# Kernel optimization log

Measured on AMD Instinct MI355X. Metric: run time of the kernel, lower is better.

## Reference

```python
import jax, jax.numpy as jnp
import numpy as np

DIM = 128
NHEADS = 8
N = 4096
ALPHA = 0.2  # LeakyReLU negative slope
EPS = 1e-5   # LayerNorm eps


def setup_inputs() -> dict:
    key = jax.random.key(0)
    ks = jax.random.split(key, 8)
    s = 1.0 / np.sqrt(DIM)
    nodes = jax.random.normal(ks[0], (N, DIM), dtype=jnp.float32)
    adj = jax.random.randint(ks[1], (N, N), 0, 2, dtype=jnp.int32)
    # per-head GAT params: W [H,D,D], attention vectors a1,a2 [H,D]
    W = jax.random.normal(ks[2], (NHEADS, DIM, DIM), dtype=jnp.float32) * s
    a1 = jax.random.normal(ks[3], (NHEADS, DIM), dtype=jnp.float32) * s
    a2 = jax.random.normal(ks[4], (NHEADS, DIM), dtype=jnp.float32) * s
    # linear1: (dim*nheads) -> dim
    W1 = jax.random.normal(ks[5], (NHEADS * DIM, DIM), dtype=jnp.float32) * (1.0 / np.sqrt(NHEADS * DIM))
    b1 = jnp.zeros((DIM,), dtype=jnp.float32)
    gamma = jnp.ones((DIM,), dtype=jnp.float32)
    beta = jnp.zeros((DIM,), dtype=jnp.float32)
    return {"nodes": nodes, "adj": adj, "W": W, "a1": a1, "a2": a2,
            "W1": W1, "b1": b1, "gamma": gamma, "beta": beta}


def _layernorm(x, gamma, beta):
    mu = jnp.mean(x, axis=-1, keepdims=True)
    var = jnp.mean((x - mu) ** 2, axis=-1, keepdims=True)
    return (x - mu) * jax.lax.rsqrt(var + EPS) * gamma + beta


def reference(nodes, adj, W, a1, a2, W1, b1, gamma, beta):
    # Eval mode: all dropouts are identity.
    # Multi-head GAT: Wh [H, N, D]
    Wh = jnp.einsum('nd,hde->hne', nodes, W)
    f1 = jnp.einsum('hnd,hd->hn', Wh, a1)   # [H, N]
    f2 = jnp.einsum('hnd,hd->hn', Wh, a2)   # [H, N]
    e = jax.nn.leaky_relu(f1[:, :, None] + f2[:, None, :], negative_slope=ALPHA)  # [H,N,N]
    mask = (adj > 0)[None, :, :]
    att = jnp.where(mask, e, jnp.float32(-9e15))
    att = jax.nn.softmax(att, axis=-1)
    h = jnp.einsum('hnm,hmd->hnd', att, Wh)  # [H, N, D]
    h = jax.nn.elu(h)
    # concat heads along feature dim -> [N, H*D]
    cat = jnp.transpose(h, (1, 0, 2)).reshape(N, NHEADS * DIM)
    x = jax.nn.elu(cat @ W1 + b1)            # [N, D]
    out = _layernorm(nodes + x, gamma, beta)
    return out
```

## Files before the change

kernel.cpp:

```cpp
#include <hip/hip_runtime.h>
#include <hip/hip_bf16.h>


#define NN 4096
#define ALPHA 0.2f
#define EPSLN 1e-5f
#define LOG2E 1.4426950408889634f

typedef __attribute__((ext_vector_type(8))) _Float16 f16x8;
typedef __attribute__((ext_vector_type(4))) _Float16 f16x4;
typedef __attribute__((ext_vector_type(2))) _Float16 f16x2;
typedef __attribute__((ext_vector_type(4))) float f32x4;
typedef __attribute__((ext_vector_type(4))) int i32x4;
typedef __fp16 h16x2 __attribute__((ext_vector_type(2)));

union F16x8 { f16x8 v; f16x2 h[4]; unsigned u[4]; };
union F16x4 { f16x4 v; f16x2 h[2]; };
union PKU { f16x2 f; unsigned u; h16x2 r; };

static __device__ inline f16x2 pkrtz(float a, float b) {
  union { decltype(__builtin_amdgcn_cvt_pkrtz(0.f, 0.f)) r; f16x2 h; } u;
  u.r = __builtin_amdgcn_cvt_pkrtz(a, b);
  return u.h;
}

#if __has_builtin(__builtin_amdgcn_exp2f)
#define EXP2(x) __builtin_amdgcn_exp2f(x)
#else
#define EXP2(x) exp2f(x)
#endif

static __device__ __forceinline__ unsigned pk_mul(unsigned a, unsigned b) {
  unsigned d;
  asm("v_pk_mul_f16 %0, %1, %2" : "=v"(d) : "v"(a), "v"(b));
  return d;
}
static __device__ __forceinline__ unsigned pk_max(unsigned a, unsigned b) {
  unsigned d;
  asm("v_pk_max_f16 %0, %1, %2" : "=v"(d) : "v"(a), "v"(b));
  return d;
}

static __device__ __forceinline__ float fdot2u(unsigned a, unsigned b, float c) {
#if __has_builtin(__builtin_amdgcn_fdot2)
  PKU ua, ub; ua.u = a; ub.u = b;
  return __builtin_amdgcn_fdot2(ua.r, ub.r, c, false);
#else
  PKU ua, ub; ua.u = a; ub.u = b;
  return c + (float)ua.f[0] * (float)ub.f[0] + (float)ua.f[1] * (float)ub.f[1];
#endif
}

static __device__ __forceinline__ void gload16(const void* g, void* l) {
  __builtin_amdgcn_global_load_lds(
      (const __attribute__((address_space(1))) void*)g,
      (__attribute__((address_space(3))) void*)l, 16, 0, 0);
}

static __device__ inline unsigned long long sp4(unsigned long long x) {
  x = (x | (x << 24)) & 0x000000FF000000FFULL;
  x = (x | (x << 12)) & 0x000F000F000F000FULL;
  x = (x | (x << 6))  & 0x0303030303030303ULL;
  x = (x | (x << 3))  & 0x1111111111111111ULL;
  return x;
}

__global__ void k_packprep(const int* __restrict__ adj, unsigned long long* __restrict__ maskT,
                           const float* __restrict__ W, const float* __restrict__ W1,
                           _Float16* __restrict__ Wt, _Float16* __restrict__ W1t) {
  int bid = blockIdx.x;
  if (bid < 16384) {
    int wv = threadIdx.x >> 6, l = threadIdx.x & 63;
    int gid = bid * 4 + wv;
    int row = gid >> 4, chunk = gid & 15;
    i32x4 v = *(const i32x4*)(adj + ((size_t)row << 12) + chunk * 256 + l * 4);
    unsigned long long b0 = __ballot(v.x > 0);
    unsigned long long b1 = __ballot(v.y > 0);
    unsigned long long b2 = __ballot(v.z > 0);
    unsigned long long b3 = __ballot(v.w > 0);
    if (l < 4) {
      int sh = l * 16;
      unsigned long long w = sp4((b0 >> sh) & 0xFFFF)
                           | (sp4((b1 >> sh) & 0xFFFF) << 1)
                           | (sp4((b2 >> sh) & 0xFFFF) << 2)
                           | (sp4((b3 >> sh) & 0xFFFF) << 3);
      maskT[(size_t)(chunk * 4 + l) * NN + row] = w;
    }
  } else {
    int idx = (bid - 16384) * 256 + threadIdx.x;
    if (idx < 131072) {
      int h = idx >> 14, r = idx & 16383, d = r >> 7, e = r & 127;
      Wt[h * 16384 + e * 128 + d] = (_Float16)W[idx];
    } else {
      int j = idx - 131072;
      int k = j >> 7, d = j & 127;
      W1t[d * 1024 + k] = (_Float16)W1[j];
    }
  }
}

__global__ __launch_bounds__(256) void k_wh(const float* __restrict__ nodes,
    const _Float16* __restrict__ Wt, const float* __restrict__ a1,
    const float* __restrict__ a2, _Float16* __restrict__ Whbt,
    float* __restrict__ f1L, float* __restrict__ f2L) {
  int h = blockIdx.y;
  int wv = threadIdx.x >> 6, l = threadIdx.x & 63;
  int lr = l & 15, lg = l >> 4;
  int ibase = blockIdx.x * 64 + wv * 16;
  f32x4 acc[8] = {};
  const float* arow = nodes + (size_t)(ibase + lr) * 128;
  const _Float16* bbase = Wt + h * 16384;
#pragma unroll
  for (int ks = 0; ks < 4; ++ks) {
    int k0 = ks * 32 + lg * 8;
    f32x4 av0 = *(const f32x4*)(arow + k0);
    f32x4 av1 = *(const f32x4*)(arow + k0 + 4);
    F16x8 A;
    A.h[0] = pkrtz(av0[0], av0[1]);
    A.h[1] = pkrtz(av0[2], av0[3]);
    A.h[2] = pkrtz(av1[0], av1[1]);
    A.h[3] = pkrtz(av1[2], av1[3]);
#pragma unroll
    for (int nt = 0; nt < 8; ++nt) {
      f16x8 B = *(const f16x8*)(bbase + (nt * 16 + lr) * 128 + k0);
      acc[nt] = __builtin_amdgcn_mfma_f32_16x16x32_f16(A.v, B, acc[nt], 0, 0, 0);
    }
  }
#pragma unroll
  for (int nt = 0; nt < 8; ++nt) {
    F16x4 o;
    o.h[0] = pkrtz(acc[nt][0], acc[nt][1]);
    o.h[1] = pkrtz(acc[nt][2], acc[nt][3]);
    *(f16x4*)(Whbt + (size_t)(h * 128 + nt * 16 + lr) * NN + ibase + lg * 4) = o.v;
  }
  float a1r[8], a2r[8];
#pragma unroll
  for (int nt = 0; nt < 8; ++nt) {
    a1r[nt] = a1[h * 128 + nt * 16 + lr];
    a2r[nt] = a2[h * 128 + nt * 16 + lr];
  }
#pragma unroll
  for (int r = 0; r < 4; ++r) {
    float s1 = 0.f, s2 = 0.f;
#pragma unroll
    for (int nt = 0; nt < 8; ++nt) { s1 += acc[nt][r] * a1r[nt]; s2 += acc[nt][r] * a2r[nt]; }
    s1 += __shfl_xor(s1, 1, 16); s1 += __shfl_xor(s1, 2, 16);
    s1 += __shfl_xor(s1, 4, 16); s1 += __shfl_xor(s1, 8, 16);
    s2 += __shfl_xor(s2, 1, 16); s2 += __shfl_xor(s2, 2, 16);
    s2 += __shfl_xor(s2, 4, 16); s2 += __shfl_xor(s2, 8, 16);
    if (lr == 0) {
      int i = ibase + lg * 4 + r;
      f1L[h * NN + i] = s1 * LOG2E;
      f2L[h * NN + i] = s2 * LOG2E;
    }
  }
}

__global__ __launch_bounds__(1024) void k_m2(const float* __restrict__ f2L,
    float* __restrict__ M2L, _Float16* __restrict__ e2ph) {
  __shared__ float red[16];
  int h = blockIdx.x, t = threadIdx.x;
  float a[4];
#pragma unroll
  for (int i = 0; i < 4; ++i) a[i] = f2L[h * NN + t + i * 1024];
  float v = fmaxf(fmaxf(a[0], a[1]), fmaxf(a[2], a[3]));
#pragma unroll
  for (int off = 1; off < 64; off <<= 1) v = fmaxf(v, __shfl_xor(v, off, 64));
  if ((t & 63) == 0) red[t >> 6] = v;
  __syncthreads();
  if (t < 16) {
    float m = red[t];
#pragma unroll
    for (int off = 1; off < 16; off <<= 1) m = fmaxf(m, __shfl_xor(m, off, 16));
    if (t == 0) { red[0] = m; M2L[h] = m; }
  }
  __syncthreads();
  float M2 = red[0];
#pragma unroll
  for (int i = 0; i < 4; ++i) {
    float d = a[i] - M2;
    e2ph[h * 8192 + t + i * 1024] = (_Float16)EXP2(d);
    e2ph[h * 8192 + 4096 + t + i * 1024] = (_Float16)EXP2(ALPHA * d);
  }
}

__global__ __launch_bounds__(256, 2) void k_attn(const _Float16* __restrict__ Whbt,
    const float* __restrict__ f1L, const float* __restrict__ M2L,
    const _Float16* __restrict__ e2ph, const unsigned long long* __restrict__ maskT,
    _Float16* __restrict__ hcat) {
  __shared__ __align__(16) char Bt[2][32768];
  __shared__ __align__(16) _Float16 e2s[2][256];
  __shared__ float denL[4][64];
  int t = threadIdx.x, jq = t >> 6, l = t & 63, lr = l & 15, lg = l >> 4;
  int bid = blockIdx.x;
  int h = bid & 7;
  int rowbase = (bid >> 3) * 64;
  float M2 = M2L[h];
  unsigned E1u[4], Eau[4];
  int rg[4];
#pragma unroll
  for (int g = 0; g < 4; ++g) {
    rg[g] = rowbase + g * 16 + lr;
    float f1 = f1L[h * NN + rg[g]];
    float s = f1 + M2;
    float mL = fmaxf(s, ALPHA * s);
    float e1 = EXP2(s - mL), ea = EXP2(ALPHA * s - mL);
    PKU p1; p1.f = pkrtz(e1, e1); E1u[g] = p1.u;
    PKU p2; p2.f = pkrtz(ea, ea); Eau[g] = p2.u;
  }
  f32x4 acc[4][8] = {};
  float den[4] = {};
  const _Float16* src = Whbt + ((size_t)h << 19);
  const _Float16* ept = e2ph + h * 8192;

  int t4 = t >> 4;
  int jc = (t & 15) ^ (t4 & 15);
  size_t goff = (size_t)t4 * NN + jc * 8;
  size_t gE = (size_t)(((t >> 4) & 1) * 4096) + (t & 15) * 8;
  int mshift = (jq & 1) * 32 + lg * 8;
  int wbase = jq >> 1;

  unsigned long long mc[4];
#pragma unroll
  for (int g = 0; g < 4; ++g) mc[g] = maskT[(size_t)wbase * NN + rg[g]];
  {
    const _Float16* gp = src + goff;
    char* lb = &Bt[0][0] + t * 16;
#pragma unroll
    for (int p = 0; p < 8; ++p)
      gload16(gp + (size_t)p * 16 * NN, lb + p * 4096);
    if (t < 32) gload16(ept + gE, (char*)&e2s[0][0] + t * 16);
  }
  __syncthreads();

  for (int ct = 0; ct < 32; ++ct) {
    unsigned long long mn[4] = {};
    if (ct + 1 < 32) {
#pragma unroll
      for (int g = 0; g < 4; ++g)
        mn[g] = maskT[(size_t)((ct + 1) * 2 + wbase) * NN + rg[g]];
      const _Float16* gp = src + goff + (ct + 1) * 128;
      char* lb = &Bt[(ct + 1) & 1][0] + t * 16;
#pragma unroll
      for (int p = 0; p < 8; ++p)
        gload16(gp + (size_t)p * 16 * NN, lb + p * 4096);
      if (t < 32) gload16(ept + gE + (ct + 1) * 128, (char*)&e2s[(ct + 1) & 1][0] + t * 16);
    }
    const char* btr = &Bt[ct & 1][0];
    const char* e2p = (const char*)&e2s[ct & 1][0];
    i32x4 e2w = *(const i32x4*)(e2p + jq * 64 + lg * 16);
    i32x4 e2aw = *(const i32x4*)(e2p + 256 + jq * 64 + lg * 16);
    F16x8 afr[4];
#pragma unroll
    for (int g = 0; g < 4; ++g) {
      unsigned bits = (unsigned)(mc[g] >> mshift) & 0xFFu;
      float dg = den[g];
#pragma unroll
      for (int pi = 0; pi < 4; ++pi) {
        unsigned mx = pk_max(pk_mul(E1u[g], (unsigned)e2w[pi]),
                             pk_mul(Eau[g], (unsigned)e2aw[pi]));
        unsigned b = (bits >> (2 * pi)) & 3u;
        mx &= ((b & 1u) ? 0x0000FFFFu : 0u) | ((b & 2u) ? 0xFFFF0000u : 0u);
        afr[g].u[pi] = mx;
        dg = fdot2u(mx, 0x3C003C00u, dg);
      }
      den[g] = dg;
    }
    __builtin_amdgcn_s_setprio(1);
#pragma unroll
    for (int nt = 0; nt < 8; ++nt) {
      int d = nt * 16 + lr;
      int byteoff = d * 256 + (((jq * 4 + lg) ^ lr) << 4);
      f16x8 B = *(const f16x8*)(btr + byteoff);
#pragma unroll
      for (int g = 0; g < 4; ++g)
        acc[g][nt] = __builtin_amdgcn_mfma_f32_16x16x32_f16(afr[g].v, B, acc[g][nt], 0, 0, 0);
    }
    __builtin_amdgcn_s_setprio(0);
    __syncthreads();
#pragma unroll
    for (int g = 0; g < 4; ++g) mc[g] = mn[g];
  }
#pragma unroll
  for (int g = 0; g < 4; ++g) {
    den[g] += __shfl_xor(den[g], 16, 64);
    den[g] += __shfl_xor(den[g], 32, 64);
  }
  if (l < 16) {
#pragma unroll
    for (int g = 0; g < 4; ++g) denL[jq][g * 16 + lr] = den[g];
  }

  float* cmb = (float*)Bt;
#pragma unroll
  for (int ph = 0; ph < 4; ++ph) {
    if (jq == ph) {
      if (ph == 0) {
#pragma unroll
        for (int g = 0; g < 4; ++g)
#pragma unroll
          for (int nt = 0; nt < 8; ++nt)
#pragma unroll
            for (int r = 0; r < 4; ++r)
              cmb[(g * 16 + lg * 4 + r) * 132 + nt * 16 + lr] = acc[g][nt][r];
      } else {
#pragma unroll
        for (int g = 0; g < 4; ++g)
#pragma unroll
          for (int nt = 0; nt < 8; ++nt)
#pragma unroll
            for (int r = 0; r < 4; ++r)
              cmb[(g * 16 + lg * 4 + r) * 132 + nt * 16 + lr] += acc[g][nt][r];
      }
    }
    __syncthreads();
  }
  {
    int row = t >> 2, seg = t & 3;
    const float* rgp = cmb + row * 132 + seg * 32;
    float dsum = denL[0][row] + denL[1][row] + denL[2][row] + denL[3][row];
    float rc = __builtin_amdgcn_rcpf(dsum);
    _Float16* outp = hcat + (size_t)(rowbase + row) * 1024 + h * 128 + seg * 32;
#pragma unroll
    for (int q8 = 0; q8 < 4; ++q8) {
      f32x4 va = *(const f32x4*)(rgp + q8 * 8);
      f32x4 vb = *(const f32x4*)(rgp + q8 * 8 + 4);
      float x[8];
#pragma unroll
      for (int c = 0; c < 4; ++c) { x[c] = va[c] * rc; x[4 + c] = vb[c] * rc; }
#pragma unroll
      for (int c = 0; c < 8; ++c) x[c] = x[c] > 0.f ? x[c] : EXP2(x[c] * LOG2E) - 1.f;
      F16x8 o;
      o.h[0] = pkrtz(x[0], x[1]); o.h[1] = pkrtz(x[2], x[3]);
      o.h[2] = pkrtz(x[4], x[5]); o.h[3] = pkrtz(x[6], x[7]);
      *(f16x8*)(outp + q8 * 8) = o.v;
    }
  }
}

__global__ __launch_bounds__(256) void k_out(const _Float16* __restrict__ hcat,
    const _Float16* __restrict__ W1t, const float* __restrict__ b1,
    const float* __restrict__ nodes, const float* __restrict__ gamma,
    const float* __restrict__ beta, float* __restrict__ out) {
  __shared__ __align__(16) float part[4][16][132];
  int t = threadIdx.x, w = t >> 6, l = t & 63, lr = l & 15, lg = l >> 4;
  int ibase = blockIdx.x * 16;
  f32x4 acc[8] = {};
  const _Float16* arow = hcat + (size_t)(ibase + lr) * 1024 + w * 256;
  const _Float16* bb = W1t + w * 256;
#pragma unroll
  for (int ks = 0; ks < 8; ++ks) {
    int k0 = ks * 32 + lg * 8;
    f16x8 A = *(const f16x8*)(arow + k0);
#pragma unroll
    for (int nt = 0; nt < 8; ++nt) {
      f16x8 B = *(const f16x8*)(bb + (nt * 16 + lr) * 1024 + k0);
      acc[nt] = __builtin_amdgcn_mfma_f32_16x16x32_f16(A, B, acc[nt], 0, 0, 0);
    }
  }
#pragma unroll
  for (int nt = 0; nt < 8; ++nt)
#pragma unroll
    for (int r = 0; r < 4; ++r)
      part[w][lg * 4 + r][nt * 16 + lr] = acc[nt][r];
  __syncthreads();
  int row = t >> 4, c16 = t & 15;
  int d0 = c16 * 8;
  size_t gi = (size_t)(ibase + row) * 128;
  f32x4 pa = {}, pb = {};
#pragma unroll
  for (int q = 0; q < 4; ++q) {
    pa += *(const f32x4*)&part[q][row][d0];
    pb += *(const f32x4*)&part[q][row][d0 + 4];
  }
  f32x4 ba = *(const f32x4*)(b1 + d0), bbv = *(const f32x4*)(b1 + d0 + 4);
  f32x4 na = *(const f32x4*)(nodes + gi + d0), nb = *(const f32x4*)(nodes + gi + d0 + 4);
  float y[8];
  float sum = 0.f, sq = 0.f;
#pragma unroll
  for (int c = 0; c < 4; ++c) {
    float x = pa[c] + ba[c];
    x = x > 0.f ? x : EXP2(x * LOG2E) - 1.f;
    y[c] = x + na[c];
    float x2 = pb[c] + bbv[c];
    x2 = x2 > 0.f ? x2 : EXP2(x2 * LOG2E) - 1.f;
    y[4 + c] = x2 + nb[c];
  }
#pragma unroll
  for (int c = 0; c < 8; ++c) { sum += y[c]; sq += y[c] * y[c]; }
#pragma unroll
  for (int off = 1; off < 16; off <<= 1) {
    sum += __shfl_xor(sum, off, 16);
    sq += __shfl_xor(sq, off, 16);
  }
  float mu = sum * (1.f / 128.f);
  float var = sq * (1.f / 128.f) - mu * mu;
  float rs = __builtin_amdgcn_rsqf(var + EPSLN);
  f32x4 ga = *(const f32x4*)(gamma + d0), gb = *(const f32x4*)(gamma + d0 + 4);
  f32x4 bea = *(const f32x4*)(beta + d0), beb = *(const f32x4*)(beta + d0 + 4);
  f32x4 o0, o1;
#pragma unroll
  for (int c = 0; c < 4; ++c) {
    o0[c] = (y[c] - mu) * rs * ga[c] + bea[c];
    o1[c] = (y[4 + c] - mu) * rs * gb[c] + beb[c];
  }
  *(f32x4*)(out + gi + d0) = o0;
  *(f32x4*)(out + gi + d0 + 4) = o1;
}

extern "C" void kernel_launch(void* const* d_in, const int* in_sizes, int n_in,
                              void* d_out, int out_size, void* d_ws, size_t ws_size,
                              hipStream_t stream) {
  const float* nodes = (const float*)d_in[0];
  const int* adj = (const int*)d_in[1];
  const float* W = (const float*)d_in[2];
  const float* a1 = (const float*)d_in[3];
  const float* a2 = (const float*)d_in[4];
  const float* W1 = (const float*)d_in[5];
  const float* b1 = (const float*)d_in[6];
  const float* gamma = (const float*)d_in[7];
  const float* beta = (const float*)d_in[8];
  float* out = (float*)d_out;
  char* ws = (char*)d_ws;

  const size_t OFF_MASK = 0;
  const size_t OFF_WHBT = 2097152;
  const size_t OFF_F1 = OFF_WHBT + 8388608;
  const size_t OFF_F2 = OFF_F1 + 131072;
  const size_t OFF_M2 = OFF_F2 + 131072;
  const size_t OFF_E2T = OFF_M2 + 256;
  const size_t OFF_WT = OFF_E2T + 131072;
  const size_t OFF_W1T = OFF_WT + 262144;
  const size_t OFF_HCAT = OFF_W1T + 262144;

  unsigned long long* maskT = (unsigned long long*)(ws + OFF_MASK);
  _Float16* Whbt = (_Float16*)(ws + OFF_WHBT);
  float* f1L = (float*)(ws + OFF_F1);
  float* f2L = (float*)(ws + OFF_F2);
  float* M2L = (float*)(ws + OFF_M2);
  _Float16* e2ph = (_Float16*)(ws + OFF_E2T);
  _Float16* Wt = (_Float16*)(ws + OFF_WT);
  _Float16* W1t = (_Float16*)(ws + OFF_W1T);
  _Float16* hcat = (_Float16*)(ws + OFF_HCAT);

  k_packprep<<<17408, 256, 0, stream>>>(adj, maskT, W, W1, Wt, W1t);
  k_wh<<<dim3(64, 8), 256, 0, stream>>>(nodes, Wt, a1, a2, Whbt, f1L, f2L);
  k_m2<<<8, 1024, 0, stream>>>(f2L, M2L, e2ph);
  k_attn<<<512, 256, 0, stream>>>(Whbt, f1L, M2L, e2ph, maskT, hcat);
  k_out<<<256, 256, 0, stream>>>(hcat, W1t, b1, nodes, gamma, beta, out);
}
```

Measured before the change: 92.90 us.

## Enlarge attention tile to 128 rows and 256-column K-chunks with 512-thread blocks

The attention kernel now uses 512-thread blocks that each cover 128 query rows, split as two row halves by four K-quarter waves. Each K-chunk grows to 256 columns, and the XOR swizzle on the shared-memory Wh tile is adjusted to match. Every loaded Wh tile is now reused across twice as many rows, and the loop runs half as many iterations with half as many barriers. In exchange, the block uses about 128KB of LDS double buffer, which probably allows only one block per CU despite the launch bound of 2. The grid also drops to 256 blocks, which lowers occupancy and latency hiding.

```diff
diff --git a/kernel.cpp b/kernel.cpp
--- a/kernel.cpp
+++ b/kernel.cpp
@@ -184,23 +184,24 @@
   }
 }
 
-__global__ __launch_bounds__(256, 2) void k_attn(const _Float16* __restrict__ Whbt,
+__global__ __launch_bounds__(512, 2) void k_attn(const _Float16* __restrict__ Whbt,
     const float* __restrict__ f1L, const float* __restrict__ M2L,
     const _Float16* __restrict__ e2ph, const unsigned long long* __restrict__ maskT,
     _Float16* __restrict__ hcat) {
-  __shared__ __align__(16) char Bt[2][32768];
-  __shared__ __align__(16) _Float16 e2s[2][256];
-  __shared__ float denL[4][64];
-  int t = threadIdx.x, jq = t >> 6, l = t & 63, lr = l & 15, lg = l >> 4;
+  __shared__ __align__(16) char Bt[2][65536];
+  __shared__ __align__(16) _Float16 e2s[2][512];
+  __shared__ float denL[4][128];
+  int t = threadIdx.x, w = t >> 6, l = t & 63, lr = l & 15, lg = l >> 4;
+  int rh = w >> 2, q = w & 3;
   int bid = blockIdx.x;
   int h = bid & 7;
-  int rowbase = (bid >> 3) * 64;
+  int rowbase = (bid >> 3) * 128;
   float M2 = M2L[h];
   unsigned E1u[4], Eau[4];
   int rg[4];
 #pragma unroll
   for (int g = 0; g < 4; ++g) {
-    rg[g] = rowbase + g * 16 + lr;
+    rg[g] = rowbase + rh * 64 + g * 16 + lr;
     float f1 = f1L[h * NN + rg[g]];
     float s = f1 + M2;
     float mL = fmaxf(s, ALPHA * s);
@@ -213,70 +214,76 @@
   const _Float16* src = Whbt + ((size_t)h << 19);
   const _Float16* ept = e2ph + h * 8192;
 
-  int t4 = t >> 4;
-  int jc = (t & 15) ^ (t4 & 15);
-  size_t goff = (size_t)t4 * NN + jc * 8;
-  size_t gE = (size_t)(((t >> 4) & 1) * 4096) + (t & 15) * 8;
-  int mshift = (jq & 1) * 32 + lg * 8;
-  int wbase = jq >> 1;
+  int tr = t >> 5;
+  int jc0 = (t & 31) ^ tr;
+  const _Float16* gp[8];
+#pragma unroll
+  for (int p = 0; p < 8; ++p) {
+    int jc = jc0 ^ ((p & 1) << 4);
+    gp[p] = src + ((size_t)(p * 16 + tr) << 12) + jc * 8;
+  }
+  const _Float16* egp = ept + ((t >> 5) & 1) * 4096 + (t & 31) * 8;
 
   unsigned long long mc[4];
 #pragma unroll
-  for (int g = 0; g < 4; ++g) mc[g] = maskT[(size_t)wbase * NN + rg[g]];
+  for (int g = 0; g < 4; ++g) mc[g] = maskT[(size_t)q * NN + rg[g]];
   {
-    const _Float16* gp = src + goff;
     char* lb = &Bt[0][0] + t * 16;
 #pragma unroll
-    for (int p = 0; p < 8; ++p)
-      gload16(gp + (size_t)p * 16 * NN, lb + p * 4096);
-    if (t < 32) gload16(ept + gE, (char*)&e2s[0][0] + t * 16);
+    for (int p = 0; p < 8; ++p) gload16(gp[p], lb + p * 8192);
+    if (t < 64) gload16(egp, (char*)&e2s[0][0] + t * 16);
   }
   __syncthreads();
 
-  for (int ct = 0; ct < 32; ++ct) {
+#pragma unroll 2
+  for (int ct = 0; ct < 16; ++ct) {
+    int cur = ct & 1;
     unsigned long long mn[4] = {};
-    if (ct + 1 < 32) {
+    if (ct + 1 < 16) {
 #pragma unroll
       for (int g = 0; g < 4; ++g)
-        mn[g] = maskT[(size_t)((ct + 1) * 2 + wbase) * NN + rg[g]];
-      const _Float16* gp = src + goff + (ct + 1) * 128;
-      char* lb = &Bt[(ct + 1) & 1][0] + t * 16;
+        mn[g] = maskT[(size_t)((ct + 1) * 4 + q) * NN + rg[g]];
+      char* lb = &Bt[cur ^ 1][0] + t * 16;
 #pragma unroll
       for (int p = 0; p < 8; ++p)
-        gload16(gp + (size_t)p * 16 * NN, lb + p * 4096);
-      if (t < 32) gload16(ept + gE + (ct + 1) * 128, (char*)&e2s[(ct + 1) & 1][0] + t * 16);
-    }
-    const char* btr = &Bt[ct & 1][0];
-    const char* e2p = (const char*)&e2s[ct & 1][0];
-    i32x4 e2w = *(const i32x4*)(e2p + jq * 64 + lg * 16);
-    i32x4 e2aw = *(const i32x4*)(e2p + 256 + jq * 64 + lg * 16);
-    F16x8 afr[4];
-#pragma unroll
-    for (int g = 0; g < 4; ++g) {
-      unsigned bits = (unsigned)(mc[g] >> mshift) & 0xFFu;
-      float dg = den[g];
-#pragma unroll
-      for (int pi = 0; pi < 4; ++pi) {
-        unsigned mx = pk_max(pk_mul(E1u[g], (unsigned)e2w[pi]),
-                             pk_mul(Eau[g], (unsigned)e2aw[pi]));
-        unsigned b = (bits >> (2 * pi)) & 3u;
-        mx &= ((b & 1u) ? 0x0000FFFFu : 0u) | ((b & 2u) ? 0xFFFF0000u : 0u);
-        afr[g].u[pi] = mx;
-        dg = fdot2u(mx, 0x3C003C00u, dg);
+        gload16(gp[p] + (size_t)(ct + 1) * 256, lb + p * 8192);
+      if (t < 64) gload16(egp + (size_t)(ct + 1) * 256, (char*)&e2s[cur ^ 1][0] + t * 16);
+    }
+    const char* btr = &Bt[cur][0];
+    const _Float16* e2p = &e2s[cur][0];
+#pragma unroll
+    for (int ks = 0; ks < 2; ++ks) {
+      i32x4 e2w = *(const i32x4*)(e2p + q * 64 + ks * 32 + lg * 8);
+      i32x4 e2aw = *(const i32x4*)(e2p + 256 + q * 64 + ks * 32 + lg * 8);
+      F16x8 afr[4];
+#pragma unroll
+      for (int g = 0; g < 4; ++g) {
+        unsigned bits = (unsigned)(mc[g] >> (ks * 32 + lg * 8)) & 0xFFu;
+        float dg = den[g];
+#pragma unroll
+        for (int pi = 0; pi < 4; ++pi) {
+          unsigned mx = pk_max(pk_mul(E1u[g], (unsigned)e2w[pi]),
+                               pk_mul(Eau[g], (unsigned)e2aw[pi]));
+          unsigned b = (bits >> (2 * pi)) & 3u;
+          mx &= ((b & 1u) ? 0x0000FFFFu : 0u) | ((b & 2u) ? 0xFFFF0000u : 0u);
+          afr[g].u[pi] = mx;
+          dg = fdot2u(mx, 0x3C003C00u, dg);
+        }
+        den[g] = dg;
       }
-      den[g] = dg;
-    }
-    __builtin_amdgcn_s_setprio(1);
-#pragma unroll
-    for (int nt = 0; nt < 8; ++nt) {
-      int d = nt * 16 + lr;
-      int byteoff = d * 256 + (((jq * 4 + lg) ^ lr) << 4);
-      f16x8 B = *(const f16x8*)(btr + byteoff);
-#pragma unroll
-      for (int g = 0; g < 4; ++g)
-        acc[g][nt] = __builtin_amdgcn_mfma_f32_16x16x32_f16(afr[g].v, B, acc[g][nt], 0, 0, 0);
-    }
-    __builtin_amdgcn_s_setprio(0);
+      int s0 = q * 8 + ks * 4 + lg;
+      __builtin_amdgcn_s_setprio(1);
+#pragma unroll
+      for (int nt = 0; nt < 8; ++nt) {
+        int d = nt * 16 + lr;
+        int byteoff = d * 512 + ((s0 ^ (d & 31)) << 4);
+        f16x8 B = *(const f16x8*)(btr + byteoff);
+#pragma unroll
+        for (int g = 0; g < 4; ++g)
+          acc[g][nt] = __builtin_amdgcn_mfma_f32_16x16x32_f16(afr[g].v, B, acc[g][nt], 0, 0, 0);
+      }
+      __builtin_amdgcn_s_setprio(0);
+    }
     __syncthreads();
 #pragma unroll
     for (int g = 0; g < 4; ++g) mc[g] = mn[g];
@@ -288,13 +295,13 @@
   }
   if (l < 16) {
 #pragma unroll
-    for (int g = 0; g < 4; ++g) denL[jq][g * 16 + lr] = den[g];
+    for (int g = 0; g < 4; ++g) denL[q][rh * 64 + g * 16 + lr] = den[g];
   }
 
   float* cmb = (float*)Bt;
 #pragma unroll
   for (int ph = 0; ph < 4; ++ph) {
-    if (jq == ph) {
+    if (q == ph) {
       if (ph == 0) {
 #pragma unroll
         for (int g = 0; g < 4; ++g)
@@ -302,7 +309,7 @@
           for (int nt = 0; nt < 8; ++nt)
 #pragma unroll
             for (int r = 0; r < 4; ++r)
-              cmb[(g * 16 + lg * 4 + r) * 132 + nt * 16 + lr] = acc[g][nt][r];
+              cmb[(rh * 64 + g * 16 + lg * 4 + r) * 132 + nt * 16 + lr] = acc[g][nt][r];
       } else {
 #pragma unroll
         for (int g = 0; g < 4; ++g)
@@ -310,7 +317,7 @@
           for (int nt = 0; nt < 8; ++nt)
 #pragma unroll
             for (int r = 0; r < 4; ++r)
-              cmb[(g * 16 + lg * 4 + r) * 132 + nt * 16 + lr] += acc[g][nt][r];
+              cmb[(rh * 64 + g * 16 + lg * 4 + r) * 132 + nt * 16 + lr] += acc[g][nt][r];
       }
     }
     __syncthreads();
@@ -369,9 +376,9 @@
   size_t gi = (size_t)(ibase + row) * 128;
   f32x4 pa = {}, pb = {};
 #pragma unroll
-  for (int q = 0; q < 4; ++q) {
-    pa += *(const f32x4*)&part[q][row][d0];
-    pb += *(const f32x4*)&part[q][row][d0 + 4];
+  for (int qq = 0; qq < 4; ++qq) {
+    pa += *(const f32x4*)&part[qq][row][d0];
+    pb += *(const f32x4*)&part[qq][row][d0 + 4];
   }
   f32x4 ba = *(const f32x4*)(b1 + d0), bbv = *(const f32x4*)(b1 + d0 + 4);
   f32x4 na = *(const f32x4*)(nodes + gi + d0), nb = *(const f32x4*)(nodes + gi + d0 + 4);
@@ -446,6 +453,6 @@
   k_packprep<<<17408, 256, 0, stream>>>(adj, maskT, W, W1, Wt, W1t);
   k_wh<<<dim3(64, 8), 256, 0, stream>>>(nodes, Wt, a1, a2, Whbt, f1L, f2L);
   k_m2<<<8, 1024, 0, stream>>>(f2L, M2L, e2ph);
-  k_attn<<<512, 256, 0, stream>>>(Whbt, f1L, M2L, e2ph, maskT, hcat);
+  k_attn<<<256, 512, 0, stream>>>(Whbt, f1L, M2L, e2ph, maskT, hcat);
   k_out<<<256, 256, 0, stream>>>(hcat, W1t, b1, nodes, gamma, beta, out);
 }
```

New measurement: 126.2 us. 1.36x slower.

## Load attention B fragments directly from global into registers, drop LDS double buffer

Applied to the files above, without the earlier changes.

The attention kernel no longer stages the transposed Wh tile through a double-buffered LDS area with global_load_lds. Each wave now loads its B fragments straight from global memory into registers every iteration, and the whole per-head e2 row is preloaded into shared memory once. This removes the per-iteration __syncthreads and cuts LDS use to about 33 KB, which may allow more resident blocks. In exchange each wave issues uncoalesced-ish strided global loads with no explicit prefetch, so the MFMAs can stall on load latency, and the four waves reload B data that they previously shared.

```diff
diff --git a/kernel.cpp b/kernel.cpp
--- a/kernel.cpp
+++ b/kernel.cpp
@@ -49,12 +49,6 @@
   PKU ua, ub; ua.u = a; ub.u = b;
   return c + (float)ua.f[0] * (float)ub.f[0] + (float)ua.f[1] * (float)ub.f[1];
 #endif
-}
-
-static __device__ __forceinline__ void gload16(const void* g, void* l) {
-  __builtin_amdgcn_global_load_lds(
-      (const __attribute__((address_space(1))) void*)g,
-      (__attribute__((address_space(3))) void*)l, 16, 0, 0);
 }
 
 static __device__ inline unsigned long long sp4(unsigned long long x) {
@@ -188,10 +182,10 @@
     const float* __restrict__ f1L, const float* __restrict__ M2L,
     const _Float16* __restrict__ e2ph, const unsigned long long* __restrict__ maskT,
     _Float16* __restrict__ hcat) {
-  __shared__ __align__(16) char Bt[2][32768];
-  __shared__ __align__(16) _Float16 e2s[2][256];
+  __shared__ __align__(16) char shm[33792];
   __shared__ float denL[4][64];
-  int t = threadIdx.x, jq = t >> 6, l = t & 63, lr = l & 15, lg = l >> 4;
+  _Float16* e2s = (_Float16*)shm;
+  int t = threadIdx.x, q = t >> 6, l = t & 63, lr = l & 15, lg = l >> 4;
   int bid = blockIdx.x;
   int h = bid & 7;
   int rowbase = (bid >> 3) * 64;
@@ -213,25 +207,21 @@
   const _Float16* src = Whbt + ((size_t)h << 19);
   const _Float16* ept = e2ph + h * 8192;
 
-  int t4 = t >> 4;
-  int jc = (t & 15) ^ (t4 & 15);
-  size_t goff = (size_t)t4 * NN + jc * 8;
-  size_t gE = (size_t)(((t >> 4) & 1) * 4096) + (t & 15) * 8;
-  int mshift = (jq & 1) * 32 + lg * 8;
-  int wbase = jq >> 1;
+#pragma unroll
+  for (int p = 0; p < 4; ++p) {
+    int c = t + p * 256;
+    *(f16x8*)(e2s + c * 8) = *(const f16x8*)(ept + c * 8);
+  }
+  __syncthreads();
+
+  int jbase = q * 32 + lg * 8;
+  int wbase = q >> 1;
+  int mshift = (q & 1) * 32 + lg * 8;
+  const _Float16* bsrc = src + jbase;
 
   unsigned long long mc[4];
 #pragma unroll
   for (int g = 0; g < 4; ++g) mc[g] = maskT[(size_t)wbase * NN + rg[g]];
-  {
-    const _Float16* gp = src + goff;
-    char* lb = &Bt[0][0] + t * 16;
-#pragma unroll
-    for (int p = 0; p < 8; ++p)
-      gload16(gp + (size_t)p * 16 * NN, lb + p * 4096);
-    if (t < 32) gload16(ept + gE, (char*)&e2s[0][0] + t * 16);
-  }
-  __syncthreads();
 
   for (int ct = 0; ct < 32; ++ct) {
     unsigned long long mn[4] = {};
@@ -239,17 +229,15 @@
 #pragma unroll
       for (int g = 0; g < 4; ++g)
         mn[g] = maskT[(size_t)((ct + 1) * 2 + wbase) * NN + rg[g]];
-      const _Float16* gp = src + goff + (ct + 1) * 128;
-      char* lb = &Bt[(ct + 1) & 1][0] + t * 16;
-#pragma unroll
-      for (int p = 0; p < 8; ++p)
-        gload16(gp + (size_t)p * 16 * NN, lb + p * 4096);
-      if (t < 32) gload16(ept + gE + (ct + 1) * 128, (char*)&e2s[(ct + 1) & 1][0] + t * 16);
-    }
-    const char* btr = &Bt[ct & 1][0];
-    const char* e2p = (const char*)&e2s[ct & 1][0];
-    i32x4 e2w = *(const i32x4*)(e2p + jq * 64 + lg * 16);
-    i32x4 e2aw = *(const i32x4*)(e2p + 256 + jq * 64 + lg * 16);
+    }
+    const _Float16* bp = bsrc + ct * 128 + (size_t)lr * NN;
+    f16x8 Bfr[8];
+#pragma unroll
+    for (int nt = 0; nt < 8; ++nt)
+      Bfr[nt] = *(const f16x8*)(bp + (size_t)nt * 16 * NN);
+    const _Float16* e2l = e2s + ct * 128 + jbase;
+    i32x4 e2w = *(const i32x4*)e2l;
+    i32x4 e2aw = *(const i32x4*)(e2l + 4096);
     F16x8 afr[4];
 #pragma unroll
     for (int g = 0; g < 4; ++g) {
@@ -268,16 +256,11 @@
     }
     __builtin_amdgcn_s_setprio(1);
 #pragma unroll
-    for (int nt = 0; nt < 8; ++nt) {
-      int d = nt * 16 + lr;
-      int byteoff = d * 256 + (((jq * 4 + lg) ^ lr) << 4);
-      f16x8 B = *(const f16x8*)(btr + byteoff);
+    for (int nt = 0; nt < 8; ++nt)
 #pragma unroll
       for (int g = 0; g < 4; ++g)
-        acc[g][nt] = __builtin_amdgcn_mfma_f32_16x16x32_f16(afr[g].v, B, acc[g][nt], 0, 0, 0);
-    }
+        acc[g][nt] = __builtin_amdgcn_mfma_f32_16x16x32_f16(afr[g].v, Bfr[nt], acc[g][nt], 0, 0, 0);
     __builtin_amdgcn_s_setprio(0);
-    __syncthreads();
 #pragma unroll
     for (int g = 0; g < 4; ++g) mc[g] = mn[g];
   }
@@ -286,15 +269,17 @@
     den[g] += __shfl_xor(den[g], 16, 64);
     den[g] += __shfl_xor(den[g], 32, 64);
   }
+  __syncthreads();
   if (l < 16) {
 #pragma unroll
-    for (int g = 0; g < 4; ++g) denL[jq][g * 16 + lr] = den[g];
-  }
-
-  float* cmb = (float*)Bt;
+    for (int g = 0; g < 4; ++g) denL[q][g * 16 + lr] = den[g];
+  }
+
+  float* cmb = (float*)shm;
 #pragma unroll
   for (int ph = 0; ph < 4; ++ph) {
-    if (jq == ph) {
+    __syncthreads();
+    if (q == ph) {
       if (ph == 0) {
 #pragma unroll
         for (int g = 0; g < 4; ++g)
@@ -313,8 +298,8 @@
               cmb[(g * 16 + lg * 4 + r) * 132 + nt * 16 + lr] += acc[g][nt][r];
       }
     }
-    __syncthreads();
-  }
+  }
+  __syncthreads();
   {
     int row = t >> 2, seg = t & 3;
     const float* rgp = cmb + row * 132 + seg * 32;
@@ -369,9 +354,9 @@
   size_t gi = (size_t)(ibase + row) * 128;
   f32x4 pa = {}, pb = {};
 #pragma unroll
-  for (int q = 0; q < 4; ++q) {
-    pa += *(const f32x4*)&part[q][row][d0];
-    pb += *(const f32x4*)&part[q][row][d0 + 4];
+  for (int qq = 0; qq < 4; ++qq) {
+    pa += *(const f32x4*)&part[qq][row][d0];
+    pb += *(const f32x4*)&part[qq][row][d0 + 4];
   }
   f32x4 ba = *(const f32x4*)(b1 + d0), bbv = *(const f32x4*)(b1 + d0 + 4);
   f32x4 na = *(const f32x4*)(nodes + gi + d0), nb = *(const f32x4*)(nodes + gi + d0 + 4);
```

Result: slower. 119.6 us (+28.7%).
